# Kernel tuning notes

Measured on AMD Instinct MI355X. Metric: run time of the kernel, lower is better.

## Reference

```python
import jax, jax.numpy as jnp
import numpy as np

B, M, R = 1024, 2048, 8192  # batch of states, metabolites, reactions
SPARSITY = 0.002            # ~4 nonzero substrates / products per reaction


def setup_inputs() -> dict:
    key = jax.random.key(0)
    k1, k2, k3, k4, k5, k6 = jax.random.split(key, 6)
    # concentrations must be strictly positive (log used in power-law eval)
    conc = jax.random.uniform(k1, (B, M), minval=1e-3, maxval=1.0, dtype=jnp.float32)
    # sparse kinetic-order (exponent) matrix: ~4 substrates/reaction, order 1 or 2
    e_mask = jax.random.bernoulli(k2, SPARSITY, (M, R))
    E = jnp.where(e_mask, jax.random.randint(k3, (M, R), 1, 3), 0).astype(jnp.int32)
    # sparse stoichiometry matrix with coefficients in {-2,-1,1,2}
    s_mask = jax.random.bernoulli(k4, SPARSITY, (M, R))
    s_raw = jax.random.randint(k5, (M, R), 0, 4)
    s_val = jnp.where(s_raw < 2, s_raw - 2, s_raw - 1)  # {-2,-1,1,2}
    S = jnp.where(s_mask, s_val, 0).astype(jnp.int32)
    # per-reaction rate constants (the learned ParameterDict)
    k = jax.random.uniform(k6, (R,), minval=0.1, maxval=2.0, dtype=jnp.float32)
    return {"conc": conc, "E": E, "S": S, "k": k}


def reference(conc, E, S, k):
    # mass-action rate laws: v_j = k_j * prod_i c_i^{E_ij}, evaluated in log-space
    # logc: [B, M]; Ef: [M, R] -> v: [B, R]
    logc = jnp.log(conc)
    Ef = E.astype(conc.dtype)
    v = k * jnp.exp(jnp.einsum('bm,mr->br', logc, Ef))
    # stoichiometric ODE RHS: dX/dt = v @ S^T -> [B, M]
    Sf = S.astype(conc.dtype)
    dXdt = jnp.einsum('br,mr->bm', v, Sf)
    return dXdt
```

## Files before the change

kernel.cpp:

```cpp
#include <hip/hip_runtime.h>
#include <hip/hip_fp16.h>

#define Bsz 1024
#define Mm  2048
#define Rr  8192
#define EMAX 32
#define SMAX 64

typedef unsigned short ushort_t;

__global__ __launch_bounds__(256) void zero_ecnt(int* __restrict__ p) {
    p[blockIdx.x * 256 + threadIdx.x] = 0;
}

__global__ __launch_bounds__(256) void prep_kernel(
    const float* __restrict__ conc, const int* __restrict__ E, const int* __restrict__ S,
    __half2* __restrict__ logcTh2, int* __restrict__ ecnt, ushort_t* __restrict__ elist,
    int* __restrict__ scnt, ushort_t* __restrict__ slist)
{
    __shared__ float tile[64][65];
    __shared__ int nS, nE;
    __shared__ int bufS[256];
    __shared__ int bufE[256];
    const int bid = blockIdx.x;
    const int t   = threadIdx.x;

    if (bid < 512) {
        const int mt = (bid & 31) * 64;
        const int bt = (bid >> 5) * 64;
        const int lm = t & 63;
        const int w  = t >> 6;
        for (int i = w; i < 64; i += 4)
            tile[lm][i] = __logf(conc[(size_t)(bt + i) * Mm + mt + lm]);
        __syncthreads();
        const int s       = bt >> 7;
        const int colbase = (bt & 127) >> 1;
        __half2* dst = logcTh2 + (size_t)s * (Mm * 64);
        for (int idx = t; idx < 64 * 32; idx += 256) {
            const int j = idx >> 5, bp = idx & 31;
            dst[(mt + j) * 64 + colbase + bp] =
                __floats2half2_rn(tile[j][2 * bp], tile[j][2 * bp + 1]);
        }
    } else {
        const int m = bid - 512;
        if (t == 0) { nS = 0; nE = 0; }
        __syncthreads();
        const int4* S4 = (const int4*)S + (size_t)m * 2048;
        const int4* E4 = (const int4*)E + (size_t)m * 2048;
        int4 sv[8], ev[8];
        #pragma unroll
        for (int u = 0; u < 8; ++u) sv[u] = S4[t + 256 * u];
        #pragma unroll
        for (int u = 0; u < 8; ++u) ev[u] = E4[t + 256 * u];
        #pragma unroll
        for (int u = 0; u < 8; ++u) {
            const int r0 = (t + 256 * u) << 2;
            int v[4] = {sv[u].x, sv[u].y, sv[u].z, sv[u].w};
            #pragma unroll
            for (int q = 0; q < 4; ++q)
                if (v[q]) {
                    int i = atomicAdd(&nS, 1);
                    if (i < 256) bufS[i] = ((v[q] + 2) << 13) | (r0 + q);
                }
        }
        #pragma unroll
        for (int u = 0; u < 8; ++u) {
            const int r0 = (t + 256 * u) << 2;
            int v[4] = {ev[u].x, ev[u].y, ev[u].z, ev[u].w};
            #pragma unroll
            for (int q = 0; q < 4; ++q)
                if (v[q]) {
                    int i = atomicAdd(&nE, 1);
                    if (i < 256) bufE[i] = (v[q] << 13) | (r0 + q);
                }
        }
        __syncthreads();
        const int sn = min(nS, SMAX);
        if (t == 0) scnt[m] = sn;
        if (t < SMAX)
            slist[m * SMAX + t] = (t < sn) ? (ushort_t)bufS[t]
                                           : (ushort_t)0x4000;
        const int en = min(nE, 256);
        if (t < en) {
            int wv = bufE[t];
            int r  = wv & 0x1FFF;
            int e  = wv >> 13;
            int slot = atomicAdd(&ecnt[r], 1);
            if (slot < EMAX) elist[r * EMAX + slot] = (ushort_t)((e << 11) | m);
        }
    }
}

__global__ __launch_bounds__(256) void rates_kernel(
    const __half2* __restrict__ logcTh2, const float* __restrict__ kvec,
    const int* __restrict__ ecnt, const ushort_t* __restrict__ elist,
    __half2* __restrict__ VTh)
{
    const int s   = blockIdx.x & 7;
    const int rch = blockIdx.x >> 3;
    const int col = threadIdx.x & 63;
    const int wr  = __builtin_amdgcn_readfirstlane(threadIdx.x >> 6);
    const __half2* lc = logcTh2 + (size_t)s * (Mm * 64);
    __half2* vt = VTh + (size_t)s * (Rr * 64);
    const int rb = rch * 32 + wr * 8;

    int  cnt[8]; int2 L0[8]; float kk[8];
    #pragma unroll
    for (int i = 0; i < 8; ++i) {
        const int r = rb + i;
        cnt[i] = ecnt[r];
        L0[i]  = *(const int2*)(elist + (r << 5));
        kk[i]  = kvec[r];
    }
    float2 acc[8];
    unsigned w; float2 g; float v0, v1;
    #define EG2(word, c0, c1, A)                                               \
        w = (unsigned)(word);                                                  \
        v0 = (c0) ? (float)((w & 0xFFFF) >> 11) : 0.f;                         \
        v1 = (c1) ? (float)(w >> 27) : 0.f;                                    \
        g = __half22float2(lc[(w & 0x7FF) * 64 + col]);                        \
        A.x += v0 * g.x;  A.y += v0 * g.y;                                     \
        g = __half22float2(lc[((w >> 16) & 0x7FF) * 64 + col]);                \
        A.x += v1 * g.x;  A.y += v1 * g.y;
    #pragma unroll
    for (int i = 0; i < 8; ++i) {
        acc[i] = make_float2(0.f, 0.f);
        EG2(L0[i].x, cnt[i] > 0, cnt[i] > 1, acc[i])
        EG2(L0[i].y, cnt[i] > 2, cnt[i] > 3, acc[i])
    }
    #pragma unroll
    for (int i = 0; i < 8; ++i) {
        for (int j = 4; j < cnt[i]; j += 4) {
            int2 T = *(const int2*)(elist + ((rb + i) << 5) + j);
            EG2(T.x, j + 0 < cnt[i], j + 1 < cnt[i], acc[i])
            EG2(T.y, j + 2 < cnt[i], j + 3 < cnt[i], acc[i])
        }
    }
    #undef EG2
    #pragma unroll
    for (int i = 0; i < 8; ++i)
        vt[(rb + i) * 64 + col] =
            __floats2half2_rn(kk[i] * __expf(acc[i].x), kk[i] * __expf(acc[i].y));
}

__global__ __launch_bounds__(256) void assemble_kernel(
    const __half2* __restrict__ VTh, const int* __restrict__ scnt,
    const ushort_t* __restrict__ slist, float* __restrict__ out)
{
    __shared__ float tile[128][17];
    const int s   = blockIdx.x & 7;
    const int mch = blockIdx.x >> 3;
    const int col = threadIdx.x & 63;
    const int wm  = __builtin_amdgcn_readfirstlane(threadIdx.x >> 6);
    const __half2* vt = VTh + (size_t)s * (Rr * 64);
    const int m0 = mch * 16;

    int scn[4]; int4 W0[4], W1[4];
    #pragma unroll
    for (int i = 0; i < 4; ++i) {
        const int m = m0 + i * 4 + wm;
        scn[i] = scnt[m];
        W0[i]  = *(const int4*)(slist + (m << 6));
        W1[i]  = *(const int4*)(slist + (m << 6) + 8);
    }
    unsigned w; float2 v; float sw;
    #define SG(word, A)                                                        \
        w = (unsigned)(word);                                                  \
        v = __half22float2(vt[(w & 0x1FFF) * 64 + col]);                       \
        sw = (float)((int)((w & 0xFFFF) >> 13) - 2);                           \
        A.x += sw * v.x;  A.y += sw * v.y;                                     \
        v = __half22float2(vt[((w >> 16) & 0x1FFF) * 64 + col]);               \
        sw = (float)((int)(w >> 29) - 2);                                      \
        A.x += sw * v.x;  A.y += sw * v.y;
    #pragma unroll
    for (int i = 0; i < 4; ++i) {
        const int ml = i * 4 + wm;
        float2 a = make_float2(0.f, 0.f);
        SG(W0[i].x, a) SG(W0[i].y, a) SG(W0[i].z, a) SG(W0[i].w, a)
        SG(W1[i].x, a) SG(W1[i].y, a) SG(W1[i].z, a) SG(W1[i].w, a)
        for (int j = 16; j < scn[i]; j += 8) {
            int4 T = *(const int4*)(slist + ((m0 + ml) << 6) + j);
            SG(T.x, a) SG(T.y, a) SG(T.z, a) SG(T.w, a)
        }
        tile[2 * col][ml]     = a.x;
        tile[2 * col + 1][ml] = a.y;
    }
    #undef SG
    __syncthreads();
    #pragma unroll
    for (int pass = 0; pass < 2; ++pass) {
        const int bl = (threadIdx.x >> 2) + pass * 64;
        const int fl = threadIdx.x & 3;
        float4 vv = *(const float4*)&tile[bl][fl * 4];
        *(float4*)(out + (size_t)(s * 128 + bl) * Mm + m0 + fl * 4) = vv;
    }
}

extern "C" void kernel_launch(void* const* d_in, const int* in_sizes, int n_in,
                              void* d_out, int out_size, void* d_ws, size_t ws_size,
                              hipStream_t stream) {
    const float* conc = (const float*)d_in[0];
    const int*   E    = (const int*)d_in[1];
    const int*   S    = (const int*)d_in[2];
    const float* kvec = (const float*)d_in[3];
    float* out = (float*)d_out;

    __half2* VTh     = (__half2*)d_ws;
    __half2* logcTh2 = (__half2*)((char*)d_ws + (size_t)Rr * Bsz * sizeof(__half));
    int*    ecnt     = (int*)((char*)logcTh2 + (size_t)Mm * Bsz * sizeof(__half));
    int*    scnt     = ecnt + Rr;
    ushort_t* elist  = (ushort_t*)(scnt + Mm);
    ushort_t* slist  = elist + Rr * EMAX;
    const size_t need = (size_t)Rr * Bsz * sizeof(__half)
                      + (size_t)Mm * Bsz * sizeof(__half)
                      + (size_t)(Rr + Mm) * sizeof(int)
                      + (size_t)(Rr * EMAX + Mm * SMAX) * sizeof(ushort_t);
    if (ws_size < need) return;

    zero_ecnt<<<32, 256, 0, stream>>>(ecnt);
    prep_kernel<<<2560, 256, 0, stream>>>(conc, E, S, logcTh2, ecnt, elist, scnt, slist);
    rates_kernel<<<2048, 256, 0, stream>>>(logcTh2, kvec, ecnt, elist, VTh);
    assemble_kernel<<<1024, 256, 0, stream>>>(VTh, scnt, slist, out);
}
```

Before: 183.3 us.

## Build sparse lists with grid-wide strided scan and global atomics

Replaces the per-metabolite block scan, which staged nonzeros in shared memory, with a grid-wide coalesced scan. Each thread walks strided int4 chunks of E and S and pushes nonzeros straight into the global lists with global atomics. The zero-fill kernel is extended to pre-fill slist with padding and clear scnt, and consumers clamp counts to the list capacity. The aim is to remove block-level serialization and shared-memory atomics and improve load balance across the dense matrix reads, at the cost of more global atomic traffic and a nondeterministic order within each list.

```diff
diff --git a/kernel.cpp b/kernel.cpp
--- a/kernel.cpp
+++ b/kernel.cpp
@@ -9,8 +9,13 @@
 
 typedef unsigned short ushort_t;
 
-__global__ __launch_bounds__(256) void zero_ecnt(int* __restrict__ p) {
-    p[blockIdx.x * 256 + threadIdx.x] = 0;
+__global__ __launch_bounds__(256) void zero_fill(
+    unsigned* __restrict__ slist_u, int* __restrict__ ecnt, int* __restrict__ scnt)
+{
+    const int tid = blockIdx.x * 256 + threadIdx.x;
+    if (tid < 65536)       slist_u[tid] = 0x40004000u;
+    else if (tid < 73728)  ecnt[tid - 65536] = 0;
+    else                   scnt[tid - 73728] = 0;
 }
 
 __global__ __launch_bounds__(256) void prep_kernel(
@@ -19,9 +24,6 @@
     int* __restrict__ scnt, ushort_t* __restrict__ slist)
 {
     __shared__ float tile[64][65];
-    __shared__ int nS, nE;
-    __shared__ int bufS[256];
-    __shared__ int bufE[256];
     const int bid = blockIdx.x;
     const int t   = threadIdx.x;
 
@@ -42,51 +44,42 @@
                 __floats2half2_rn(tile[j][2 * bp], tile[j][2 * bp + 1]);
         }
     } else {
-        const int m = bid - 512;
-        if (t == 0) { nS = 0; nE = 0; }
-        __syncthreads();
-        const int4* S4 = (const int4*)S + (size_t)m * 2048;
-        const int4* E4 = (const int4*)E + (size_t)m * 2048;
-        int4 sv[8], ev[8];
+        const int gl = (bid - 512) * 256 + t;
+        const int4* E4 = (const int4*)E;
         #pragma unroll
-        for (int u = 0; u < 8; ++u) sv[u] = S4[t + 256 * u];
+        for (int i = 0; i < 8; ++i) {
+            const unsigned idx4 = i * 524288u + gl;
+            const int4 v = E4[idx4];
+            if (v.x | v.y | v.z | v.w) {
+                const int ib = (int)(idx4 << 2);
+                const int m = ib >> 13, r0 = ib & 8191;
+                int vv[4] = {v.x, v.y, v.z, v.w};
+                #pragma unroll
+                for (int q = 0; q < 4; ++q)
+                    if (vv[q]) {
+                        int slot = atomicAdd(&ecnt[r0 + q], 1);
+                        if (slot < EMAX)
+                            elist[(r0 + q) * EMAX + slot] = (ushort_t)((vv[q] << 11) | m);
+                    }
+            }
+        }
+        const int4* S4 = (const int4*)S;
         #pragma unroll
-        for (int u = 0; u < 8; ++u) ev[u] = E4[t + 256 * u];
-        #pragma unroll
-        for (int u = 0; u < 8; ++u) {
-            const int r0 = (t + 256 * u) << 2;
-            int v[4] = {sv[u].x, sv[u].y, sv[u].z, sv[u].w};
-            #pragma unroll
-            for (int q = 0; q < 4; ++q)
-                if (v[q]) {
-                    int i = atomicAdd(&nS, 1);
-                    if (i < 256) bufS[i] = ((v[q] + 2) << 13) | (r0 + q);
-                }
-        }
-        #pragma unroll
-        for (int u = 0; u < 8; ++u) {
-            const int r0 = (t + 256 * u) << 2;
-            int v[4] = {ev[u].x, ev[u].y, ev[u].z, ev[u].w};
-            #pragma unroll
-            for (int q = 0; q < 4; ++q)
-                if (v[q]) {
-                    int i = atomicAdd(&nE, 1);
-                    if (i < 256) bufE[i] = (v[q] << 13) | (r0 + q);
-                }
-        }
-        __syncthreads();
-        const int sn = min(nS, SMAX);
-        if (t == 0) scnt[m] = sn;
-        if (t < SMAX)
-            slist[m * SMAX + t] = (t < sn) ? (ushort_t)bufS[t]
-                                           : (ushort_t)0x4000;
-        const int en = min(nE, 256);
-        if (t < en) {
-            int wv = bufE[t];
-            int r  = wv & 0x1FFF;
-            int e  = wv >> 13;
-            int slot = atomicAdd(&ecnt[r], 1);
-            if (slot < EMAX) elist[r * EMAX + slot] = (ushort_t)((e << 11) | m);
+        for (int i = 0; i < 8; ++i) {
+            const unsigned idx4 = i * 524288u + gl;
+            const int4 v = S4[idx4];
+            if (v.x | v.y | v.z | v.w) {
+                const int ib = (int)(idx4 << 2);
+                const int m = ib >> 13, r0 = ib & 8191;
+                int vv[4] = {v.x, v.y, v.z, v.w};
+                #pragma unroll
+                for (int q = 0; q < 4; ++q)
+                    if (vv[q]) {
+                        int slot = atomicAdd(&scnt[m], 1);
+                        if (slot < SMAX)
+                            slist[m * SMAX + slot] = (ushort_t)(((vv[q] + 2) << 13) | (r0 + q));
+                    }
+            }
         }
     }
 }
@@ -108,7 +101,7 @@
     #pragma unroll
     for (int i = 0; i < 8; ++i) {
         const int r = rb + i;
-        cnt[i] = ecnt[r];
+        cnt[i] = min(ecnt[r], EMAX);
         L0[i]  = *(const int2*)(elist + (r << 5));
         kk[i]  = kvec[r];
     }
@@ -159,7 +152,7 @@
     #pragma unroll
     for (int i = 0; i < 4; ++i) {
         const int m = m0 + i * 4 + wm;
-        scn[i] = scnt[m];
+        scn[i] = min(scnt[m], SMAX);
         W0[i]  = *(const int4*)(slist + (m << 6));
         W1[i]  = *(const int4*)(slist + (m << 6) + 8);
     }
@@ -217,7 +210,7 @@
                       + (size_t)(Rr * EMAX + Mm * SMAX) * sizeof(ushort_t);
     if (ws_size < need) return;
 
-    zero_ecnt<<<32, 256, 0, stream>>>(ecnt);
+    zero_fill<<<296, 256, 0, stream>>>((unsigned*)slist, ecnt, scnt);
     prep_kernel<<<2560, 256, 0, stream>>>(conc, E, S, logcTh2, ecnt, elist, scnt, slist);
     rates_kernel<<<2048, 256, 0, stream>>>(logcTh2, kvec, ecnt, elist, VTh);
     assemble_kernel<<<1024, 256, 0, stream>>>(VTh, scnt, slist, out);
```

After: 187.0 us. 2.0% more time.
